# Kernel optimization log

Measured on AMD Instinct MI355X. Metric: run time of the kernel, lower is better.

## Reference

```python
import jax, jax.numpy as jnp
import numpy as np

V, C, H, W, RM, RD = 16, 16, 1024, 1024, 8, 4


def _cpx(x):
    # last dim 2 = (real, imag) -> complex64
    return jax.lax.complex(x[..., 0], x[..., 1])


def setup_inputs() -> dict:
    key = jax.random.key(0)
    ks = jax.random.split(key, 12)
    rn = lambda k, s, sc=1.0: jax.random.normal(k, s, dtype=jnp.float32) * sc
    ASYM = 0.01
    exp_init = jnp.array([2.0, 0.0], dtype=jnp.float32)  # exponents_initial_value_(real,imag)
    return {
        "base": rn(ks[0], (H, W, 2)),
        "mod_u": rn(ks[1], (C, H, RM, 2), 0.35),
        "mod_v": rn(ks[2], (C, RM, W, 2), 0.35),
        "del_u": rn(ks[3], (C, H, RD, 2), 0.35),
        "del_v": rn(ks[4], (C, RD, W, 2), 0.35),
        "exp_base": exp_init + rn(ks[5], (2,), ASYM),
        "exp_mod": exp_init[None, :] + rn(ks[6], (C, 2), ASYM),
        "exp_del": exp_init[None, :] + rn(ks[7], (C, 2), ASYM),
        "bias": rn(ks[8], (C, 2)),
        "scale": rn(ks[9], (C, 2)),
        "coef": rn(ks[10], (V, C, 2)),  # uniform(-2,2) real + small imag in torch; randn ok for baseline
    }


def reference(base, mod_u, mod_v, del_u, del_v, exp_base, exp_mod, exp_del, bias, scale, coef):
    b = _cpx(base)  # [H, W] complex64
    # low-rank complex reconstructions: [C, H, W]
    mod = jnp.einsum('chr,crw->chw', _cpx(mod_u), _cpx(mod_v))
    dlt = jnp.einsum('chr,crw->chw', _cpx(del_u), _cpx(del_v))
    # trainable complex exponentiation: z**w = exp(w * log z)
    pb = jnp.exp(_cpx(exp_base) * jnp.log(b))                        # [H, W]
    pm = jnp.exp(_cpx(exp_mod)[:, None, None] * jnp.log(mod))       # [C, H, W]
    pd = jnp.exp(_cpx(exp_del)[:, None, None] * jnp.log(dlt))       # [C, H, W]
    comp = _cpx(scale)[:, None, None] * (pb[None] * pm + pd) + _cpx(bias)[:, None, None]
    # coefficient-weighted sum over C components -> [V, H, W] (avoids [V,C,H,W] materialization)
    out = jnp.einsum('vc,chw->vhw', _cpx(coef), comp)
    return jnp.stack([out.real, out.imag], axis=-1)  # [V, H, W, 2] float32
```

## Files before the change

kernel.cpp:

```cpp
#include <hip/hip_runtime.h>
#include <stdint.h>

#define NV 16
#define NC 16
#define NH 1024
#define NW 1024
#define NRM 8
#define NRD 4

typedef __attribute__((ext_vector_type(4))) _Float16 f16x4;
typedef __attribute__((ext_vector_type(2))) __fp16 fp16x2_raw;
typedef __attribute__((ext_vector_type(4))) float f32x4;
typedef __attribute__((ext_vector_type(2))) float f32x2;

#define MFMA16(a, b, c) __builtin_amdgcn_mfma_f32_16x16x16f16((a), (b), (c), 0, 0, 0)

__device__ __forceinline__ uint32_t pkh(float a, float b) {
    fp16x2_raw h = __builtin_amdgcn_cvt_pkrtz(a, b);
    return __builtin_bit_cast(uint32_t, h);
}

__device__ __forceinline__ f16x4 mk4(uint32_t lo, uint32_t hi) {
    union { uint32_t u[2]; f16x4 v; } t;
    t.u[0] = lo; t.u[1] = hi;
    return t.v;
}

__device__ __forceinline__ void cmac_pk(f32x2& t, f32x2 a, f32x2 b) {
    asm("v_pk_fma_f32 %0, %1, %2, %0 op_sel_hi:[0,1,1]"
        : "+v"(t) : "v"(a), "v"(b));
    asm("v_pk_fma_f32 %0, %1, %2, %0 op_sel:[1,1,0] op_sel_hi:[1,0,1] neg_lo:[1,0,0]"
        : "+v"(t) : "v"(a), "v"(b));
}

struct c2 { f32x2 a, b; };
__device__ __forceinline__ c2 split4(float4 v) {
    c2 r; r.a = f32x2{v.x, v.y}; r.b = f32x2{v.z, v.w}; return r;
}

__device__ __forceinline__ float atan2_rev(float y, float x) {
    float ax = fabsf(x), ay = fabsf(y);
    float mx = fmaxf(ax, ay), mn = fminf(ax, ay);
    float a = mn * __builtin_amdgcn_rcpf(mx);
    float s = a * a;
    float p =              -0.00186549f;
    p = fmaf(p, s,  0.00838003f);
    p = fmaf(p, s, -0.01852970f);
    p = fmaf(p, s,  0.03080340f);
    p = fmaf(p, s, -0.05294381f);
    p = fmaf(p, s,  0.15915132f);
    p = p * a;
    float t = (ay > ax) ? (0.25f - p) : p;
    t = (x < 0.0f) ? (0.5f - t) : t;
    return (y < 0.0f) ? -t : t;
}

#define K_B 9.06472028f
#define K_D 0.05516054f

__global__ __launch_bounds__(256)
void transpose_v(const float* __restrict__ mod_v, const float* __restrict__ del_v,
                 float* __restrict__ mvT, float* __restrict__ dvT)
{
    const int idx = blockIdx.x * 256 + threadIdx.x;
    const int c = idx >> 10, w = idx & 1023;
    float2* mt = reinterpret_cast<float2*>(mvT) + idx * NRM;
    const float2* ms = reinterpret_cast<const float2*>(mod_v) + c * NRM * NW + w;
    #pragma unroll
    for (int r = 0; r < NRM; ++r) mt[r] = ms[r * NW];
    float2* dt = reinterpret_cast<float2*>(dvT) + idx * NRD;
    const float2* dsrc = reinterpret_cast<const float2*>(del_v) + c * NRD * NW + w;
    #pragma unroll
    for (int r = 0; r < NRD; ++r) dt[r] = dsrc[r * NW];
}

struct V6 { f32x2 m0, m1, m2, m3, m4, m5, m6, m7, d0, d1, d2, d3; };

template <bool TR>
__device__ __forceinline__ V6 load_v(const float* __restrict__ mvT, const float* __restrict__ dvT,
                                     const float* __restrict__ mod_v, const float* __restrict__ del_v,
                                     int c, int w)
{
    V6 r;
    if (TR) {
        const float4* mp = reinterpret_cast<const float4*>(mvT) + (c * NW + w) * 4;
        c2 q0 = split4(mp[0]), q1 = split4(mp[1]), q2 = split4(mp[2]), q3 = split4(mp[3]);
        r.m0 = q0.a; r.m1 = q0.b; r.m2 = q1.a; r.m3 = q1.b;
        r.m4 = q2.a; r.m5 = q2.b; r.m6 = q3.a; r.m7 = q3.b;
        const float4* dp = reinterpret_cast<const float4*>(dvT) + (c * NW + w) * 2;
        c2 s0 = split4(dp[0]), s1 = split4(dp[1]);
        r.d0 = s0.a; r.d1 = s0.b; r.d2 = s1.a; r.d3 = s1.b;
    } else {
        const float2* m = reinterpret_cast<const float2*>(mod_v) + c * NRM * NW + w;
        float2 a0 = m[0], a1 = m[NW], a2 = m[2*NW], a3 = m[3*NW];
        float2 a4 = m[4*NW], a5 = m[5*NW], a6 = m[6*NW], a7 = m[7*NW];
        r.m0 = f32x2{a0.x, a0.y}; r.m1 = f32x2{a1.x, a1.y};
        r.m2 = f32x2{a2.x, a2.y}; r.m3 = f32x2{a3.x, a3.y};
        r.m4 = f32x2{a4.x, a4.y}; r.m5 = f32x2{a5.x, a5.y};
        r.m6 = f32x2{a6.x, a6.y}; r.m7 = f32x2{a7.x, a7.y};
        const float2* d = reinterpret_cast<const float2*>(del_v) + c * NRD * NW + w;
        float2 b0 = d[0], b1 = d[NW], b2 = d[2*NW], b3 = d[3*NW];
        r.d0 = f32x2{b0.x, b0.y}; r.d1 = f32x2{b1.x, b1.y};
        r.d2 = f32x2{b2.x, b2.y}; r.d3 = f32x2{b3.x, b3.y};
    }
    return r;
}

template <bool TR>
__global__ __launch_bounds__(256)
void fused_kernel(const float* __restrict__ base, const float* __restrict__ mod_u,
                  const float* __restrict__ mod_v, const float* __restrict__ del_u,
                  const float* __restrict__ del_v, const float* __restrict__ exp_base,
                  const float* __restrict__ exp_mod, const float* __restrict__ exp_del,
                  const float* __restrict__ bias_, const float* __restrict__ scale_,
                  const float* __restrict__ coef, float* __restrict__ out,
                  const float* __restrict__ mvT, const float* __restrict__ dvT)
{
    __shared__ uint32_t lds[8192];
    __shared__ float4 uA4[NC][2][4];
    __shared__ float4 uD4[NC][2][2];

    const int tid    = threadIdx.x;
    const int lane   = tid & 63;
    const int wv     = tid >> 6;
    const int wchunk = (int)(blockIdx.x & 3);
    const int hp     = (int)(blockIdx.x >> 2);
    const int w      = (wchunk << 8) | tid;
    const int h0     = hp * 2;
    const int wbase  = (wchunk << 8) | (wv << 6);

    {
        float* uAf = reinterpret_cast<float*>(uA4);
        float* uDf = reinterpret_cast<float*>(uD4);
        int i = tid;
        {
            const int c = i >> 5, rr = (i >> 4) & 1, e = i & 15;
            uAf[i] = mod_u[((c * NH) + (h0 + rr)) * (NRM * 2) + e];
        }
        i = tid + 256;
        {
            const int c = i >> 5, rr = (i >> 4) & 1, e = i & 15;
            uAf[i] = mod_u[((c * NH) + (h0 + rr)) * (NRM * 2) + e];
        }
        if (tid < 256) {
            const int c = tid >> 4, rr = (tid >> 3) & 1, e = tid & 7;
            uDf[tid] = del_u[((c * NH) + (h0 + rr)) * (NRD * 2) + e];
        }
    }
    __syncthreads();

    const int vv = lane & 15;
    const int c0 = (lane >> 4) << 2;

    const float4 cfa = *reinterpret_cast<const float4*>(coef   + (vv * NC + c0) * 2);
    const float4 cfb = *reinterpret_cast<const float4*>(coef   + (vv * NC + c0) * 2 + 4);
    const float4 sca = *reinterpret_cast<const float4*>(scale_ + c0 * 2);
    const float4 scb = *reinterpret_cast<const float4*>(scale_ + c0 * 2 + 4);
    const float4 bia = *reinterpret_cast<const float4*>(bias_  + c0 * 2);
    const float4 bib = *reinterpret_cast<const float4*>(bias_  + c0 * 2 + 4);

    float c2r0 = cfa.x*sca.x - cfa.y*sca.y, c2i0 = cfa.x*sca.y + cfa.y*sca.x;
    float c2r1 = cfa.z*sca.z - cfa.w*sca.w, c2i1 = cfa.z*sca.w + cfa.w*sca.z;
    float c2r2 = cfb.x*scb.x - cfb.y*scb.y, c2i2 = cfb.x*scb.y + cfb.y*scb.x;
    float c2r3 = cfb.z*scb.z - cfb.w*scb.w, c2i3 = cfb.z*scb.w + cfb.w*scb.z;

    const f16x4 Ar = mk4(pkh(c2r0, c2r1), pkh(c2r2, c2r3));
    const f16x4 Ai = mk4(pkh(c2i0, c2i1), pkh(c2i2, c2i3));
    const f16x4 An = mk4(pkh(-c2i0, -c2i1), pkh(-c2i2, -c2i3));

    const f16x4 Kr = mk4(pkh(cfa.x, cfa.z), pkh(cfb.x, cfb.z));
    const f16x4 Ki = mk4(pkh(cfa.y, cfa.w), pkh(cfb.y, cfb.w));
    const f16x4 Kn = mk4(pkh(-cfa.y, -cfa.w), pkh(-cfb.y, -cfb.w));

    const f16x4 Bbr = mk4(pkh(bia.x, bia.z), pkh(bib.x, bib.z));
    const f16x4 Bbi = mk4(pkh(bia.y, bia.w), pkh(bib.y, bib.w));

    const f32x4 zero4 = {0.f, 0.f, 0.f, 0.f};
    const f32x4 cr4 = MFMA16(Kr, Bbr, MFMA16(Kn, Bbi, zero4));
    const f32x4 ci4 = MFMA16(Ki, Bbr, MFMA16(Kr, Bbi, zero4));

    const float ebr = exp_base[0], ebi = exp_base[1];
    const float Ab = 0.5f * ebr, Bb = ebi * K_B, Cb = ebr, Db = ebi * K_D;
    float berr[2], beir[2];
    {
        const float2 b0 = reinterpret_cast<const float2*>(base)[(h0    ) * NW + w];
        const float2 b1 = reinterpret_cast<const float2*>(base)[(h0 + 1) * NW + w];
        const float L2b0 = __builtin_amdgcn_logf(fmaf(b0.x, b0.x, b0.y * b0.y));
        const float th0  = atan2_rev(b0.y, b0.x);
        const float L2b1 = __builtin_amdgcn_logf(fmaf(b1.x, b1.x, b1.y * b1.y));
        const float th1  = atan2_rev(b1.y, b1.x);
        berr[0] = fmaf(Ab, L2b0, -Bb * th0);
        beir[0] = fmaf(Cb, th0,   Db * L2b0);
        berr[1] = fmaf(Ab, L2b1, -Bb * th1);
        beir[1] = fmaf(Cb, th1,   Db * L2b1);
    }

    uint32_t* wlds0 = lds + (wv << 10);
    uint32_t* wlds1 = lds + 4096 + (wv << 10);
    const int swz_w = (lane >> 1) & 3;

    V6 cur = load_v<TR>(mvT, dvT, mod_v, del_v, 0, w);

    #pragma unroll 1
    for (int a = 0; a < 4; ++a) {
        uint32_t p0[4], p1[4];
        #pragma unroll
        for (int j = 0; j < 4; ++j) {
            const int c = (a << 2) | j;
            V6 nxt = load_v<TR>(mvT, dvT, mod_v, del_v, (c + 1) & 15, w);

            const float2 em = reinterpret_cast<const float2*>(exp_mod)[c];
            const float2 ed = reinterpret_cast<const float2*>(exp_del)[c];
            const float kmA = 0.5f * em.x, kmB = em.y * K_B, kmC = em.x, kmD = em.y * K_D;
            const float kdA = 0.5f * ed.x, kdB = ed.y * K_B, kdC = ed.x, kdD = ed.y * K_D;

            #pragma unroll
            for (int rr = 0; rr < 2; ++rr) {
                const c2 ua = split4(uA4[c][rr][0]);
                const c2 ub = split4(uA4[c][rr][1]);
                const c2 uc_ = split4(uA4[c][rr][2]);
                const c2 ud = split4(uA4[c][rr][3]);
                const c2 da = split4(uD4[c][rr][0]);
                const c2 db = split4(uD4[c][rr][1]);

                f32x2 tm = {0.f, 0.f};
                cmac_pk(tm, ua.a,  cur.m0); cmac_pk(tm, ua.b,  cur.m1);
                cmac_pk(tm, ub.a,  cur.m2); cmac_pk(tm, ub.b,  cur.m3);
                cmac_pk(tm, uc_.a, cur.m4); cmac_pk(tm, uc_.b, cur.m5);
                cmac_pk(tm, ud.a,  cur.m6); cmac_pk(tm, ud.b,  cur.m7);
                const float mr = tm[0], mi_ = tm[1];

                f32x2 td = {0.f, 0.f};
                cmac_pk(td, da.a, cur.d0); cmac_pk(td, da.b, cur.d1);
                cmac_pk(td, db.a, cur.d2); cmac_pk(td, db.b, cur.d3);
                const float dr = td[0], di = td[1];

                const float L2m = __builtin_amdgcn_logf(fmaf(mr, mr, mi_ * mi_));
                const float thm = atan2_rev(mi_, mr);
                const float er2 = fmaf(kmA, L2m, fmaf(-kmB, thm, berr[rr]));
                const float eir = fmaf(kmC, thm, fmaf(kmD, L2m, beir[rr]));
                const float mm  = __builtin_amdgcn_exp2f(er2);
                const float fm  = __builtin_amdgcn_fractf(eir);
                const float cv  = __builtin_amdgcn_cosf(fm);
                const float sv  = __builtin_amdgcn_sinf(fm);

                const float L2d = __builtin_amdgcn_logf(fmaf(dr, dr, di * di));
                const float thd = atan2_rev(di, dr);
                const float er2d = fmaf(kdA, L2d, -kdB * thd);
                const float eird = fmaf(kdC, thd,  kdD * L2d);
                const float md  = __builtin_amdgcn_exp2f(er2d);
                const float fd  = __builtin_amdgcn_fractf(eird);
                const float cvd = __builtin_amdgcn_cosf(fd);
                const float svd = __builtin_amdgcn_sinf(fd);

                const float Pr = fmaf(mm, cv, md * cvd);
                const float Pi = fmaf(mm, sv, md * svd);
                const uint32_t pk = pkh(Pr, Pi);
                if (rr == 0) p0[j] = pk; else p1[j] = pk;
            }
            cur = nxt;
        }
        const int s = (a ^ swz_w) << 2;
        *reinterpret_cast<uint4*>(wlds0 + (lane << 4) + s) = make_uint4(p0[0], p0[1], p0[2], p0[3]);
        *reinterpret_cast<uint4*>(wlds1 + (lane << 4) + s) = make_uint4(p1[0], p1[1], p1[2], p1[3]);
    }

    const int ar  = lane >> 4;
    const int col = lane & 15;
    float2* outp = reinterpret_cast<float2*>(out);

    #pragma unroll
    for (int rr = 0; rr < 2; ++rr) {
        const uint32_t* reg = rr ? wlds1 : wlds0;
        const int h = h0 + rr;
        #pragma unroll
        for (int g = 0; g < 4; ++g) {
            const int p = (g << 4) | col;
            const int s = (ar ^ ((p >> 1) & 3)) << 2;
            const uint4 q = *reinterpret_cast<const uint4*>(reg + (p << 4) + s);
            const f16x4 Brf = mk4(__builtin_amdgcn_perm(q.y, q.x, 0x05040100u),
                                  __builtin_amdgcn_perm(q.w, q.z, 0x05040100u));
            const f16x4 Bif = mk4(__builtin_amdgcn_perm(q.y, q.x, 0x07060302u),
                                  __builtin_amdgcn_perm(q.w, q.z, 0x07060302u));
            const f32x4 Dr = MFMA16(Ar, Brf, MFMA16(An, Bif, cr4));
            const f32x4 Di = MFMA16(Ai, Brf, MFMA16(Ar, Bif, ci4));
            const int wg = wbase + (g << 4) + col;
            const int base_idx = h * NW + wg;
            #pragma unroll
            for (int j = 0; j < 4; ++j) {
                const int v = (ar << 2) + j;
                outp[v * (NH * NW) + base_idx] = make_float2(Dr[j], Di[j]);
            }
        }
    }
}

extern "C" void kernel_launch(void* const* d_in, const int* in_sizes, int n_in,
                              void* d_out, int out_size, void* d_ws, size_t ws_size,
                              hipStream_t stream) {
    const float* base     = (const float*)d_in[0];
    const float* mod_u    = (const float*)d_in[1];
    const float* mod_v    = (const float*)d_in[2];
    const float* del_u    = (const float*)d_in[3];
    const float* del_v    = (const float*)d_in[4];
    const float* exp_base = (const float*)d_in[5];
    const float* exp_mod  = (const float*)d_in[6];
    const float* exp_del  = (const float*)d_in[7];
    const float* bias_    = (const float*)d_in[8];
    const float* scale_   = (const float*)d_in[9];
    const float* coef     = (const float*)d_in[10];
    float* outp = (float*)d_out;

    const int blocks = (NH / 2) * (NW / 256);
    const size_t mvT_floats = (size_t)NC * NW * NRM * 2;
    const size_t dvT_floats = (size_t)NC * NW * NRD * 2;
    const size_t need = (mvT_floats + dvT_floats) * sizeof(float);

    if (ws_size >= need) {
        float* mvT = (float*)d_ws;
        float* dvT = mvT + mvT_floats;
        transpose_v<<<(NC * NW) / 256, 256, 0, stream>>>(mod_v, del_v, mvT, dvT);
        fused_kernel<true><<<blocks, 256, 0, stream>>>(base, mod_u, mod_v, del_u, del_v,
                                                       exp_base, exp_mod, exp_del,
                                                       bias_, scale_, coef, outp, mvT, dvT);
    } else {
        fused_kernel<false><<<blocks, 256, 0, stream>>>(base, mod_u, mod_v, del_u, del_v,
                                                        exp_base, exp_mod, exp_del,
                                                        bias_, scale_, coef, outp,
                                                        (const float*)nullptr, (const float*)nullptr);
    }
}
```

Before: 99.17 us.

## Compute MFMA B-operand directly in registers, dropping LDS staging

Each lane now computes four components (c0..c0+3) of the power terms for a single w column, which lines up with the 16x16x16 MFMA B-fragment layout. The packed results feed the coefficient MFMAs straight from registers, so the LDS staging buffer, swizzled writes and reads, and perm unpacking are gone. Each block now covers 64 columns instead of 256, giving four times as many blocks, and launch bounds request 4 blocks per CU. The trade-off is that per-block setup (mod_u/del_u staging, coefficient prep) and the base log/atan work are now repeated across more blocks and more lanes. The software prefetch of the next component's v-vectors is also removed.

```diff
diff --git a/kernel.cpp b/kernel.cpp
--- a/kernel.cpp
+++ b/kernel.cpp
@@ -107,7 +107,7 @@
 }
 
 template <bool TR>
-__global__ __launch_bounds__(256)
+__global__ __launch_bounds__(256, 4)
 void fused_kernel(const float* __restrict__ base, const float* __restrict__ mod_u,
                   const float* __restrict__ mod_v, const float* __restrict__ del_u,
                   const float* __restrict__ del_v, const float* __restrict__ exp_base,
@@ -116,18 +116,18 @@
                   const float* __restrict__ coef, float* __restrict__ out,
                   const float* __restrict__ mvT, const float* __restrict__ dvT)
 {
-    __shared__ uint32_t lds[8192];
     __shared__ float4 uA4[NC][2][4];
     __shared__ float4 uD4[NC][2][2];
 
-    const int tid    = threadIdx.x;
-    const int lane   = tid & 63;
-    const int wv     = tid >> 6;
-    const int wchunk = (int)(blockIdx.x & 3);
-    const int hp     = (int)(blockIdx.x >> 2);
-    const int w      = (wchunk << 8) | tid;
-    const int h0     = hp * 2;
-    const int wbase  = (wchunk << 8) | (wv << 6);
+    const int tid  = threadIdx.x;
+    const int lane = tid & 63;
+    const int wv   = tid >> 6;
+    const int col  = lane & 15;
+    const int kb   = lane >> 4;
+    const int bw   = (int)(blockIdx.x & 15);
+    const int hp   = (int)(blockIdx.x >> 4);
+    const int h0   = hp * 2;
+    const int w    = (bw << 6) | (wv << 4) | col;
 
     {
         float* uAf = reinterpret_cast<float*>(uA4);
@@ -149,8 +149,8 @@
     }
     __syncthreads();
 
-    const int vv = lane & 15;
-    const int c0 = (lane >> 4) << 2;
+    const int vv = col;
+    const int c0 = kb << 2;
 
     const float4 cfa = *reinterpret_cast<const float4*>(coef   + (vv * NC + c0) * 2);
     const float4 cfb = *reinterpret_cast<const float4*>(coef   + (vv * NC + c0) * 2 + 4);
@@ -195,102 +195,74 @@
         beir[1] = fmaf(Cb, th1,   Db * L2b1);
     }
 
-    uint32_t* wlds0 = lds + (wv << 10);
-    uint32_t* wlds1 = lds + 4096 + (wv << 10);
-    const int swz_w = (lane >> 1) & 3;
-
-    V6 cur = load_v<TR>(mvT, dvT, mod_v, del_v, 0, w);
-
-    #pragma unroll 1
-    for (int a = 0; a < 4; ++a) {
-        uint32_t p0[4], p1[4];
+    float Pr[2][4], Pi[2][4];
+
+    #pragma unroll
+    for (int j = 0; j < 4; ++j) {
+        const int c = c0 | j;
+        const V6 cur = load_v<TR>(mvT, dvT, mod_v, del_v, c, w);
+
+        const float2 em = reinterpret_cast<const float2*>(exp_mod)[c];
+        const float2 ed = reinterpret_cast<const float2*>(exp_del)[c];
+        const float kmA = 0.5f * em.x, kmB = em.y * K_B, kmC = em.x, kmD = em.y * K_D;
+        const float kdA = 0.5f * ed.x, kdB = ed.y * K_B, kdC = ed.x, kdD = ed.y * K_D;
+
         #pragma unroll
-        for (int j = 0; j < 4; ++j) {
-            const int c = (a << 2) | j;
-            V6 nxt = load_v<TR>(mvT, dvT, mod_v, del_v, (c + 1) & 15, w);
-
-            const float2 em = reinterpret_cast<const float2*>(exp_mod)[c];
-            const float2 ed = reinterpret_cast<const float2*>(exp_del)[c];
-            const float kmA = 0.5f * em.x, kmB = em.y * K_B, kmC = em.x, kmD = em.y * K_D;
-            const float kdA = 0.5f * ed.x, kdB = ed.y * K_B, kdC = ed.x, kdD = ed.y * K_D;
-
-            #pragma unroll
-            for (int rr = 0; rr < 2; ++rr) {
-                const c2 ua = split4(uA4[c][rr][0]);
-                const c2 ub = split4(uA4[c][rr][1]);
-                const c2 uc_ = split4(uA4[c][rr][2]);
-                const c2 ud = split4(uA4[c][rr][3]);
-                const c2 da = split4(uD4[c][rr][0]);
-                const c2 db = split4(uD4[c][rr][1]);
-
-                f32x2 tm = {0.f, 0.f};
-                cmac_pk(tm, ua.a,  cur.m0); cmac_pk(tm, ua.b,  cur.m1);
-                cmac_pk(tm, ub.a,  cur.m2); cmac_pk(tm, ub.b,  cur.m3);
-                cmac_pk(tm, uc_.a, cur.m4); cmac_pk(tm, uc_.b, cur.m5);
-                cmac_pk(tm, ud.a,  cur.m6); cmac_pk(tm, ud.b,  cur.m7);
-                const float mr = tm[0], mi_ = tm[1];
-
-                f32x2 td = {0.f, 0.f};
-                cmac_pk(td, da.a, cur.d0); cmac_pk(td, da.b, cur.d1);
-                cmac_pk(td, db.a, cur.d2); cmac_pk(td, db.b, cur.d3);
-                const float dr = td[0], di = td[1];
-
-                const float L2m = __builtin_amdgcn_logf(fmaf(mr, mr, mi_ * mi_));
-                const float thm = atan2_rev(mi_, mr);
-                const float er2 = fmaf(kmA, L2m, fmaf(-kmB, thm, berr[rr]));
-                const float eir = fmaf(kmC, thm, fmaf(kmD, L2m, beir[rr]));
-                const float mm  = __builtin_amdgcn_exp2f(er2);
-                const float fm  = __builtin_amdgcn_fractf(eir);
-                const float cv  = __builtin_amdgcn_cosf(fm);
-                const float sv  = __builtin_amdgcn_sinf(fm);
-
-                const float L2d = __builtin_amdgcn_logf(fmaf(dr, dr, di * di));
-                const float thd = atan2_rev(di, dr);
-                const float er2d = fmaf(kdA, L2d, -kdB * thd);
-                const float eird = fmaf(kdC, thd,  kdD * L2d);
-                const float md  = __builtin_amdgcn_exp2f(er2d);
-                const float fd  = __builtin_amdgcn_fractf(eird);
-                const float cvd = __builtin_amdgcn_cosf(fd);
-                const float svd = __builtin_amdgcn_sinf(fd);
-
-                const float Pr = fmaf(mm, cv, md * cvd);
-                const float Pi = fmaf(mm, sv, md * svd);
-                const uint32_t pk = pkh(Pr, Pi);
-                if (rr == 0) p0[j] = pk; else p1[j] = pk;
-            }
-            cur = nxt;
-        }
-        const int s = (a ^ swz_w) << 2;
-        *reinterpret_cast<uint4*>(wlds0 + (lane << 4) + s) = make_uint4(p0[0], p0[1], p0[2], p0[3]);
-        *reinterpret_cast<uint4*>(wlds1 + (lane << 4) + s) = make_uint4(p1[0], p1[1], p1[2], p1[3]);
-    }
-
-    const int ar  = lane >> 4;
-    const int col = lane & 15;
+        for (int rr = 0; rr < 2; ++rr) {
+            const c2 ua  = split4(uA4[c][rr][0]);
+            const c2 ub  = split4(uA4[c][rr][1]);
+            const c2 uc_ = split4(uA4[c][rr][2]);
+            const c2 ud  = split4(uA4[c][rr][3]);
+            const c2 da  = split4(uD4[c][rr][0]);
+            const c2 db  = split4(uD4[c][rr][1]);
+
+            f32x2 tm = {0.f, 0.f};
+            cmac_pk(tm, ua.a,  cur.m0); cmac_pk(tm, ua.b,  cur.m1);
+            cmac_pk(tm, ub.a,  cur.m2); cmac_pk(tm, ub.b,  cur.m3);
+            cmac_pk(tm, uc_.a, cur.m4); cmac_pk(tm, uc_.b, cur.m5);
+            cmac_pk(tm, ud.a,  cur.m6); cmac_pk(tm, ud.b,  cur.m7);
+            const float mr = tm[0], mi_ = tm[1];
+
+            f32x2 td = {0.f, 0.f};
+            cmac_pk(td, da.a, cur.d0); cmac_pk(td, da.b, cur.d1);
+            cmac_pk(td, db.a, cur.d2); cmac_pk(td, db.b, cur.d3);
+            const float dr = td[0], di = td[1];
+
+            const float L2m = __builtin_amdgcn_logf(fmaf(mr, mr, mi_ * mi_));
+            const float thm = atan2_rev(mi_, mr);
+            const float er2 = fmaf(kmA, L2m, fmaf(-kmB, thm, berr[rr]));
+            const float eir = fmaf(kmC, thm, fmaf(kmD, L2m, beir[rr]));
+            const float mm  = __builtin_amdgcn_exp2f(er2);
+            const float fm  = __builtin_amdgcn_fractf(eir);
+            const float cv  = __builtin_amdgcn_cosf(fm);
+            const float sv  = __builtin_amdgcn_sinf(fm);
+
+            const float L2d = __builtin_amdgcn_logf(fmaf(dr, dr, di * di));
+            const float thd = atan2_rev(di, dr);
+            const float er2d = fmaf(kdA, L2d, -kdB * thd);
+            const float eird = fmaf(kdC, thd,  kdD * L2d);
+            const float md  = __builtin_amdgcn_exp2f(er2d);
+            const float fd  = __builtin_amdgcn_fractf(eird);
+            const float cvd = __builtin_amdgcn_cosf(fd);
+            const float svd = __builtin_amdgcn_sinf(fd);
+
+            Pr[rr][j] = fmaf(mm, cv, md * cvd);
+            Pi[rr][j] = fmaf(mm, sv, md * svd);
+        }
+    }
+
     float2* outp = reinterpret_cast<float2*>(out);
-
     #pragma unroll
     for (int rr = 0; rr < 2; ++rr) {
-        const uint32_t* reg = rr ? wlds1 : wlds0;
-        const int h = h0 + rr;
+        const f16x4 Brf = mk4(pkh(Pr[rr][0], Pr[rr][1]), pkh(Pr[rr][2], Pr[rr][3]));
+        const f16x4 Bif = mk4(pkh(Pi[rr][0], Pi[rr][1]), pkh(Pi[rr][2], Pi[rr][3]));
+        const f32x4 Dr = MFMA16(Ar, Brf, MFMA16(An, Bif, cr4));
+        const f32x4 Di = MFMA16(Ai, Brf, MFMA16(Ar, Bif, ci4));
+        const int bidx = (h0 + rr) * NW + w;
         #pragma unroll
-        for (int g = 0; g < 4; ++g) {
-            const int p = (g << 4) | col;
-            const int s = (ar ^ ((p >> 1) & 3)) << 2;
-            const uint4 q = *reinterpret_cast<const uint4*>(reg + (p << 4) + s);
-            const f16x4 Brf = mk4(__builtin_amdgcn_perm(q.y, q.x, 0x05040100u),
-                                  __builtin_amdgcn_perm(q.w, q.z, 0x05040100u));
-            const f16x4 Bif = mk4(__builtin_amdgcn_perm(q.y, q.x, 0x07060302u),
-                                  __builtin_amdgcn_perm(q.w, q.z, 0x07060302u));
-            const f32x4 Dr = MFMA16(Ar, Brf, MFMA16(An, Bif, cr4));
-            const f32x4 Di = MFMA16(Ai, Brf, MFMA16(Ar, Bif, ci4));
-            const int wg = wbase + (g << 4) + col;
-            const int base_idx = h * NW + wg;
-            #pragma unroll
-            for (int j = 0; j < 4; ++j) {
-                const int v = (ar << 2) + j;
-                outp[v * (NH * NW) + base_idx] = make_float2(Dr[j], Di[j]);
-            }
+        for (int jj = 0; jj < 4; ++jj) {
+            const int v = (kb << 2) + jj;
+            outp[v * (NH * NW) + bidx] = make_float2(Dr[jj], Di[jj]);
         }
     }
 }
@@ -311,7 +283,7 @@
     const float* coef     = (const float*)d_in[10];
     float* outp = (float*)d_out;
 
-    const int blocks = (NH / 2) * (NW / 256);
+    const int blocks = (NH / 2) * (NW / 64);
     const size_t mvT_floats = (size_t)NC * NW * NRM * 2;
     const size_t dvT_floats = (size_t)NC * NW * NRD * 2;
     const size_t need = (mvT_floats + dvT_floats) * sizeof(float);
```

Measured after the change: 89.42 us. -9.8%, faster.
